# Performance work log

Hardware: AMD Instinct MI355X
Metric: run time of the kernel (lower is better)

The kernel has to match this reference:

```python
import jax, jax.numpy as jnp
import numpy as np

B, L, W = 512, 1024, 256


def setup_inputs() -> dict:
    key = jax.random.key(0)
    ks = jax.random.split(key, 7)
    # spin configurations in {-1, +1}
    x = (jax.random.randint(ks[0], (B, L), 0, 2).astype(jnp.float32) * 2.0 - 1.0)
    s = 0.1  # param init scale
    w_ih = jax.random.normal(ks[1], (3 * W, 2), jnp.float32) * s
    w_hh = jax.random.normal(ks[2], (3 * W, W), jnp.float32) * s
    b_ih = jax.random.normal(ks[3], (3 * W,), jnp.float32) * s
    b_hh = jax.random.normal(ks[4], (3 * W,), jnp.float32) * s
    fc_w = jax.random.normal(ks[5], (2, W), jnp.float32) * s
    fc_b = jax.random.normal(ks[6], (2,), jnp.float32) * s
    return {"x": x, "w_ih": w_ih, "w_hh": w_hh, "b_ih": b_ih,
            "b_hh": b_hh, "fc_w": fc_w, "fc_b": fc_b}


def reference(x, w_ih, w_hh, b_ih, b_hh, fc_w, fc_b):
    b, n = x.shape
    w = w_hh.shape[1]
    mask = (1.0 + x) * 0.5                                   # [B, L]
    # input to step i is x[:, i-1]; step 0 uses x_init = 0 (embeds to [0.5, 0.5])
    xs = jnp.concatenate([jnp.zeros((b, 1), x.dtype), x[:, :-1]], axis=1)
    emb = jnp.stack([(xs + 1.0) * 0.5, 1.0 - (xs + 1.0) * 0.5], axis=-1)  # [B, L, 2]
    # precompute all input-side gate projections in one GEMM: [B, L, 3W]
    gi_all = jnp.einsum('blk,gk->blg', emb, w_ih) + b_ih

    def step(h, inp):
        gi, m = inp                                          # [B,3W], [B]
        gh = h @ w_hh.T + b_hh                               # [B,3W]
        i_r, i_z, i_n = jnp.split(gi, 3, axis=1)
        h_r, h_z, h_n = jnp.split(gh, 3, axis=1)
        r = jax.nn.sigmoid(i_r + h_r)
        z = jax.nn.sigmoid(i_z + h_z)
        ng = jnp.tanh(i_n + r * h_n)
        h_next = (1.0 - z) * ng + z * h                      # torch GRUCell update
        y = jax.nn.log_softmax(h_next @ fc_w.T + fc_b, axis=1)  # [B,2]
        lp = y[:, 0] * m + y[:, 1] * (1.0 - m)
        return h_next, lp

    gi_t = jnp.swapaxes(gi_all, 0, 1)                        # [L, B, 3W]
    m_t = mask.T                                             # [L, B]
    h0 = jnp.zeros((b, w), x.dtype)
    _, lps = jax.lax.scan(step, h0, (gi_t, m_t))             # lps: [L, B]
    return lps.sum(axis=0)                                   # [B]
```

## Files before the change

### kernel.cpp

```cpp
#include <hip/hip_runtime.h>
#include <math.h>

#define SL 1024
#define NW 256

typedef _Float16 half8 __attribute__((ext_vector_type(8)));
typedef _Float16 half2t __attribute__((ext_vector_type(2)));
typedef float f32x4 __attribute__((ext_vector_type(4)));

__device__ __forceinline__ float rcp_f(float v) { return __builtin_amdgcn_rcpf(v); }

__global__ __launch_bounds__(512, 2) void gru_mfma_kernel(
    const float* __restrict__ x, const float* __restrict__ w_ih,
    const float* __restrict__ w_hh, const float* __restrict__ b_ih,
    const float* __restrict__ b_hh, const float* __restrict__ fc_w,
    const float* __restrict__ fc_b, float* __restrict__ out)
{
    const int tid  = threadIdx.x;
    const int w    = tid >> 6;
    const int lane = tid & 63;
    const int c    = lane & 15;
    const int g    = lane >> 4;
    const int gl   = g & 1;
    const int row0 = blockIdx.x * 2;

    __shared__ float    x_lds[2][1026];
    __shared__ __align__(16) _Float16 h_lds[2][2][288];
    __shared__ float    dpart[SL][8][2];
    __shared__ float    wsum[8][2];

    for (int i = tid; i < 2 * SL; i += 512) {
        int b = i >> 10, j = i & (SL - 1);
        x_lds[b][1 + j] = (x[(size_t)(row0 + b) * SL + j] + 1.0f) * 0.5f;
    }
    if (tid < 2) x_lds[tid][0] = 0.5f;
    for (int i = tid; i < 2 * 2 * 288; i += 512)
        ((_Float16*)h_lds)[i] = (_Float16)0.0f;

    half8 Bf[6][8];
    #pragma unroll
    for (int f = 0; f < 6; ++f) {
        const int q = f >> 1, jt = f & 1;
        const int urow = q * NW + (2 * w + jt) * 16 + c;
        #pragma unroll
        for (int j = 0; j < 8; ++j) {
            const int ktp = (w + j) & 7;
            const float* p = w_hh + (size_t)urow * NW + ktp * 32 + g * 8;
            float4 lo = *(const float4*)p;
            float4 hi = *(const float4*)(p + 4);
            half8 hb;
            hb[0] = (_Float16)lo.x; hb[1] = (_Float16)lo.y;
            hb[2] = (_Float16)lo.z; hb[3] = (_Float16)lo.w;
            hb[4] = (_Float16)hi.x; hb[5] = (_Float16)hi.y;
            hb[6] = (_Float16)hi.z; hb[7] = (_Float16)hi.w;
            Bf[f][j] = hb;
        }
    }

    half8 B7 = (half8)(_Float16)0.0f;
    if (c == 0) {
        #pragma unroll
        for (int e = 0; e < 8; ++e) {
            const int k = w * 32 + g * 8 + e;
            B7[e] = (_Float16)(fc_w[k] - fc_w[NW + k]);
        }
    }

    const int u = 32 * w + 16 * gl + c;
    half2t pkr, pkz, pkn;
    {
        float w0, w1;
        w0 = w_ih[2 * u]; w1 = w_ih[2 * u + 1];
        pkr[0] = (_Float16)(w1 + b_ih[u] + b_hh[u]);
        pkr[1] = (_Float16)(w0 - w1);
        w0 = w_ih[2 * (NW + u)]; w1 = w_ih[2 * (NW + u) + 1];
        pkz[0] = (_Float16)(w1 + b_ih[NW + u] + b_hh[NW + u]);
        pkz[1] = (_Float16)(w0 - w1);
        w0 = w_ih[2 * (2 * NW + u)]; w1 = w_ih[2 * (2 * NW + u) + 1];
        pkn[0] = (_Float16)(w1 + b_ih[2 * NW + u]);
        pkn[1] = (_Float16)(w0 - w1);
    }
    const float bhn = b_hh[2 * NW + u];
    const float bd  = fc_b[0] - fc_b[1];

    const f32x4 zc = {0.f, 0.f, 0.f, 0.f};
    float h0 = 0.f, h1 = 0.f;

    __syncthreads();

    #pragma unroll 1
    for (int t = 0; t < SL; ++t) {
        const int cur = t & 1, nxt = cur ^ 1;

        f32x4 acc[6];
        f32x4 acc7;
        #pragma unroll
        for (int j = 0; j < 8; ++j) {
            const int ktp = (w + j) & 7;
            half8 A = *(const half8*)&h_lds[cur][lane & 1][ktp * 32 + g * 8];
            if (j == 0) {
                #pragma unroll
                for (int f = 0; f < 6; ++f)
                    acc[f] = __builtin_amdgcn_mfma_f32_16x16x32_f16(A, Bf[f][0], zc, 0, 0, 0);
                acc7 = __builtin_amdgcn_mfma_f32_16x16x32_f16(A, B7, zc, 0, 0, 0);
            } else {
                #pragma unroll
                for (int f = 0; f < 6; ++f)
                    acc[f] = __builtin_amdgcn_mfma_f32_16x16x32_f16(A, Bf[f][j], acc[f], 0, 0, 0);
            }
        }

        const float m0 = x_lds[0][t];
        const float m1 = x_lds[1][t];

        const float ar0 = gl ? acc[1][0] : acc[0][0];
        const float ar1 = gl ? acc[1][1] : acc[0][1];
        const float az0 = gl ? acc[3][0] : acc[2][0];
        const float az1 = gl ? acc[3][1] : acc[2][1];
        const float an0 = gl ? acc[5][0] : acc[4][0];
        const float an1 = gl ? acc[5][1] : acc[4][1];

        const float cmr = (float)pkr[0], cdr = (float)pkr[1];
        const float cmz = (float)pkz[0], cdz = (float)pkz[1];
        const float cmn = (float)pkn[0], cdn = (float)pkn[1];

        const float vr0 = ar0 + fmaf(m0, cdr, cmr);
        const float rr0 = rcp_f(1.f + __expf(-vr0));
        const float vz0 = az0 + fmaf(m0, cdz, cmz);
        const float zz0 = rcp_f(1.f + __expf(-vz0));
        const float un0 = fmaf(rr0, an0 + bhn, fmaf(m0, cdn, cmn));
        const float ng0 = fmaf(-2.f, rcp_f(1.f + __expf(2.f * un0)), 1.f);
        const float hn0 = fmaf(zz0, h0 - ng0, ng0);
        const float vr1 = ar1 + fmaf(m1, cdr, cmr);
        const float rr1 = rcp_f(1.f + __expf(-vr1));
        const float vz1 = az1 + fmaf(m1, cdz, cmz);
        const float zz1 = rcp_f(1.f + __expf(-vz1));
        const float un1 = fmaf(rr1, an1 + bhn, fmaf(m1, cdn, cmn));
        const float ng1 = fmaf(-2.f, rcp_f(1.f + __expf(2.f * un1)), 1.f);
        const float hn1 = fmaf(zz1, h1 - ng1, ng1);
        h0 = hn0; h1 = hn1;

        if (g < 2) {
            h_lds[nxt][0][u] = (_Float16)hn0;
            h_lds[nxt][1][u] = (_Float16)hn1;
        }
        if (lane == 0 && t != 0) {
            dpart[t - 1][w][0] = acc7[0];
            dpart[t - 1][w][1] = acc7[1];
        }

        __syncthreads();
    }

    {
        half8 Ah = *(const half8*)&h_lds[0][lane & 1][w * 32 + g * 8];
        f32x4 accE = __builtin_amdgcn_mfma_f32_16x16x32_f16(Ah, B7, zc, 0, 0, 0);
        if (lane == 0) {
            dpart[SL - 1][w][0] = accE[0];
            dpart[SL - 1][w][1] = accE[1];
        }
    }
    __syncthreads();

    float lpp0 = 0.f, lpp1 = 0.f;
    #pragma unroll 1
    for (int t = tid; t < SL; t += 512) {
        float d0 = bd, d1 = bd;
        #pragma unroll
        for (int q = 0; q < 8; ++q) { d0 += dpart[t][q][0]; d1 += dpart[t][q][1]; }
        const float u0 = (x_lds[0][t + 1] > 0.5f) ? -d0 : d0;
        const float u1 = (x_lds[1][t + 1] > 0.5f) ? -d1 : d1;
        lpp0 -= fmaxf(u0, 0.f) + __logf(1.f + __expf(-fabsf(u0)));
        lpp1 -= fmaxf(u1, 0.f) + __logf(1.f + __expf(-fabsf(u1)));
    }
    #pragma unroll
    for (int s = 1; s < 64; s <<= 1) {
        lpp0 += __shfl_xor(lpp0, s);
        lpp1 += __shfl_xor(lpp1, s);
    }
    if (lane == 0) { wsum[w][0] = lpp0; wsum[w][1] = lpp1; }
    __syncthreads();
    if (tid < 2) {
        float s = 0.f;
        #pragma unroll
        for (int q = 0; q < 8; ++q) s += wsum[q][tid];
        out[row0 + tid] = s;
    }
}

extern "C" void kernel_launch(void* const* d_in, const int* in_sizes, int n_in,
                              void* d_out, int out_size, void* d_ws, size_t ws_size,
                              hipStream_t stream) {
    const float* x    = (const float*)d_in[0];
    const float* w_ih = (const float*)d_in[1];
    const float* w_hh = (const float*)d_in[2];
    const float* b_ih = (const float*)d_in[3];
    const float* b_hh = (const float*)d_in[4];
    const float* fc_w = (const float*)d_in[5];
    const float* fc_b = (const float*)d_in[6];
    gru_mfma_kernel<<<256, 512, 0, stream>>>(
        x, w_ih, w_hh, b_ih, b_hh, fc_w, fc_b, (float*)d_out);
}
```

Before: 1.081 ms.

## Issue own-slice MFMA before barrier and split gate math across lane groups

Each wave's own 32-wide k-slice of h is written only by that wave. The step's first MFMA chunk, plus the fc projection, is therefore issued right after the new h is stored and before the block barrier. That work overlaps with barrier wait instead of lengthening the next step's critical path. The gate nonlinearities are also split so each lane group computes one batch row rather than both, using the replicated MFMA output rows. This halves the per-lane transcendental work in the serial recurrence. The cost is accumulators carried across iterations and reliance on wave-local LDS ordering before the barrier.

```diff
diff --git a/kernel.cpp b/kernel.cpp
--- a/kernel.cpp
+++ b/kernel.cpp
@@ -22,6 +22,7 @@
     const int c    = lane & 15;
     const int g    = lane >> 4;
     const int gl   = g & 1;
+    const int row  = g >> 1;
     const int row0 = blockIdx.x * 2;
 
     __shared__ float    x_lds[2][1026];
@@ -84,7 +85,12 @@
     const float bd  = fc_b[0] - fc_b[1];
 
     const f32x4 zc = {0.f, 0.f, 0.f, 0.f};
-    float h0 = 0.f, h1 = 0.f;
+    float h0 = 0.f;
+
+    f32x4 acc[6];
+    #pragma unroll
+    for (int f = 0; f < 6; ++f) acc[f] = zc;
+    f32x4 acc7 = zc;
 
     __syncthreads();
 
@@ -92,73 +98,55 @@
     for (int t = 0; t < SL; ++t) {
         const int cur = t & 1, nxt = cur ^ 1;
 
-        f32x4 acc[6];
-        f32x4 acc7;
-        #pragma unroll
-        for (int j = 0; j < 8; ++j) {
-            const int ktp = (w + j) & 7;
-            half8 A = *(const half8*)&h_lds[cur][lane & 1][ktp * 32 + g * 8];
-            if (j == 0) {
-                #pragma unroll
-                for (int f = 0; f < 6; ++f)
-                    acc[f] = __builtin_amdgcn_mfma_f32_16x16x32_f16(A, Bf[f][0], zc, 0, 0, 0);
-                acc7 = __builtin_amdgcn_mfma_f32_16x16x32_f16(A, B7, zc, 0, 0, 0);
-            } else {
-                #pragma unroll
-                for (int f = 0; f < 6; ++f)
-                    acc[f] = __builtin_amdgcn_mfma_f32_16x16x32_f16(A, Bf[f][j], acc[f], 0, 0, 0);
-            }
+        if (lane == 0 && t != 0) {
+            dpart[t - 1][w][0] = acc7[0];
+            dpart[t - 1][w][1] = acc7[1];
         }
 
-        const float m0 = x_lds[0][t];
-        const float m1 = x_lds[1][t];
+        const _Float16* hb = &h_lds[cur][lane & 1][g * 8];
+        #pragma unroll
+        for (int j = 1; j < 8; ++j) {
+            const int ktp = (w + j) & 7;
+            half8 A = *(const half8*)(hb + ktp * 32);
+            #pragma unroll
+            for (int f = 0; f < 6; ++f)
+                acc[f] = __builtin_amdgcn_mfma_f32_16x16x32_f16(A, Bf[f][j], acc[f], 0, 0, 0);
+        }
 
-        const float ar0 = gl ? acc[1][0] : acc[0][0];
-        const float ar1 = gl ? acc[1][1] : acc[0][1];
-        const float az0 = gl ? acc[3][0] : acc[2][0];
-        const float az1 = gl ? acc[3][1] : acc[2][1];
-        const float an0 = gl ? acc[5][0] : acc[4][0];
-        const float an1 = gl ? acc[5][1] : acc[4][1];
+        const float m  = x_lds[row][t];
+        const float ar = row ? (gl ? acc[1][1] : acc[0][1]) : (gl ? acc[1][0] : acc[0][0]);
+        const float az = row ? (gl ? acc[3][1] : acc[2][1]) : (gl ? acc[3][0] : acc[2][0]);
+        const float an = row ? (gl ? acc[5][1] : acc[4][1]) : (gl ? acc[5][0] : acc[4][0]);
 
         const float cmr = (float)pkr[0], cdr = (float)pkr[1];
         const float cmz = (float)pkz[0], cdz = (float)pkz[1];
         const float cmn = (float)pkn[0], cdn = (float)pkn[1];
 
-        const float vr0 = ar0 + fmaf(m0, cdr, cmr);
-        const float rr0 = rcp_f(1.f + __expf(-vr0));
-        const float vz0 = az0 + fmaf(m0, cdz, cmz);
-        const float zz0 = rcp_f(1.f + __expf(-vz0));
-        const float un0 = fmaf(rr0, an0 + bhn, fmaf(m0, cdn, cmn));
-        const float ng0 = fmaf(-2.f, rcp_f(1.f + __expf(2.f * un0)), 1.f);
-        const float hn0 = fmaf(zz0, h0 - ng0, ng0);
-        const float vr1 = ar1 + fmaf(m1, cdr, cmr);
-        const float rr1 = rcp_f(1.f + __expf(-vr1));
-        const float vz1 = az1 + fmaf(m1, cdz, cmz);
-        const float zz1 = rcp_f(1.f + __expf(-vz1));
-        const float un1 = fmaf(rr1, an1 + bhn, fmaf(m1, cdn, cmn));
-        const float ng1 = fmaf(-2.f, rcp_f(1.f + __expf(2.f * un1)), 1.f);
-        const float hn1 = fmaf(zz1, h1 - ng1, ng1);
-        h0 = hn0; h1 = hn1;
+        const float vr = ar + fmaf(m, cdr, cmr);
+        const float rr = rcp_f(1.f + __expf(-vr));
+        const float vz = az + fmaf(m, cdz, cmz);
+        const float zz = rcp_f(1.f + __expf(-vz));
+        const float un = fmaf(rr, an + bhn, fmaf(m, cdn, cmn));
+        const float ng = fmaf(-2.f, rcp_f(1.f + __expf(2.f * un)), 1.f);
+        const float hn = fmaf(zz, h0 - ng, ng);
+        h0 = hn;
 
-        if (g < 2) {
-            h_lds[nxt][0][u] = (_Float16)hn0;
-            h_lds[nxt][1][u] = (_Float16)hn1;
-        }
-        if (lane == 0 && t != 0) {
-            dpart[t - 1][w][0] = acc7[0];
-            dpart[t - 1][w][1] = acc7[1];
+        h_lds[nxt][row][u] = (_Float16)hn;
+
+        {
+            half8 A = *(const half8*)&h_lds[nxt][lane & 1][w * 32 + g * 8];
+            #pragma unroll
+            for (int f = 0; f < 6; ++f)
+                acc[f] = __builtin_amdgcn_mfma_f32_16x16x32_f16(A, Bf[f][0], zc, 0, 0, 0);
+            acc7 = __builtin_amdgcn_mfma_f32_16x16x32_f16(A, B7, zc, 0, 0, 0);
         }
 
         __syncthreads();
     }
 
-    {
-        half8 Ah = *(const half8*)&h_lds[0][lane & 1][w * 32 + g * 8];
-        f32x4 accE = __builtin_amdgcn_mfma_f32_16x16x32_f16(Ah, B7, zc, 0, 0, 0);
-        if (lane == 0) {
-            dpart[SL - 1][w][0] = accE[0];
-            dpart[SL - 1][w][1] = accE[1];
-        }
+    if (lane == 0) {
+        dpart[SL - 1][w][0] = acc7[0];
+        dpart[SL - 1][w][1] = acc7[1];
     }
     __syncthreads();
 
```

After: 1.060 ms. 1.02x faster.
